# Kernel optimization log

Measured on AMD Instinct MI355X. Metric: run time of the kernel, lower is better.

The kernel has to match this reference:

```python
import jax, jax.numpy as jnp
import numpy as np

N_NODES = 100000
N_EDGES = 1600000
N_FEAT = 32
HIDDEN = 96
N_GRAPHS = 2048


def setup_inputs() -> dict:
    key = jax.random.key(0)
    ks = jax.random.split(key, 16)
    x = jax.random.normal(ks[0], (N_NODES, N_FEAT), dtype=jnp.float32)
    edge_index = jax.random.randint(ks[1], (2, N_EDGES), 0, N_NODES, dtype=jnp.int64)
    batch = jnp.sort(jax.random.randint(ks[2], (N_NODES,), 0, N_GRAPHS, dtype=jnp.int64))

    def glorot(k, shape):
        lim = np.sqrt(6.0 / (shape[0] + shape[1]))
        return jax.random.uniform(k, shape, dtype=jnp.float32, minval=-lim, maxval=lim)

    return {
        "x": x, "edge_index": edge_index, "batch": batch,
        "W1": glorot(ks[3], (N_FEAT, HIDDEN)), "b1": jnp.zeros((HIDDEN,), jnp.float32),
        "W2": glorot(ks[4], (HIDDEN, HIDDEN)), "b2": jnp.zeros((HIDDEN,), jnp.float32),
        "W3": glorot(ks[5], (HIDDEN, HIDDEN)), "b3": jnp.zeros((HIDDEN,), jnp.float32),
        "W4": glorot(ks[6], (HIDDEN, HIDDEN)), "b4": jnp.zeros((HIDDEN,), jnp.float32),
        "Wf1": glorot(ks[7], (HIDDEN, 32)), "bf1": jnp.zeros((32,), jnp.float32),
        "Wf2": glorot(ks[8], (32, 1)), "bf2": jnp.zeros((1,), jnp.float32),
    }


def _gcn_norm(edge_index, num_nodes):
    # PyG GCNConv default: add self-loops, symmetric normalization D^-1/2 (A+I) D^-1/2
    loops = jnp.arange(num_nodes, dtype=edge_index.dtype)
    src = jnp.concatenate([edge_index[0], loops])
    dst = jnp.concatenate([edge_index[1], loops])
    deg = jax.ops.segment_sum(jnp.ones_like(dst, dtype=jnp.float32), dst, num_segments=num_nodes)
    dinv = jnp.where(deg > 0, jax.lax.rsqrt(jnp.where(deg > 0, deg, 1.0)), 0.0)
    norm = dinv[src] * dinv[dst]  # [E + N]
    return src, dst, norm


def _gcn_conv(x, src, dst, norm, W, b, num_nodes):
    xw = x @ W                      # [N, out]
    msg = xw[src] * norm[:, None]   # [E+N, out] gather + scale
    out = jax.ops.segment_sum(msg, dst, num_segments=num_nodes)  # scatter-add
    return out + b


def reference(x, edge_index, batch, W1, b1, W2, b2, W3, b3, W4, b4, Wf1, bf1, Wf2, bf2):
    n = x.shape[0]
    src, dst, norm = _gcn_norm(edge_index, n)
    h = jax.nn.relu(_gcn_conv(x, src, dst, norm, W1, b1, n))
    h = jax.nn.relu(_gcn_conv(h, src, dst, norm, W2, b2, n))
    h = jax.nn.relu(_gcn_conv(h, src, dst, norm, W3, b3, n))
    h = jax.nn.relu(_gcn_conv(h, src, dst, norm, W4, b4, n))
    g = jax.ops.segment_sum(h, batch, num_segments=N_GRAPHS)  # global_add_pool [G, 96]
    g = jax.nn.relu(g @ Wf1 + bf1)
    return g @ Wf2 + bf2  # [G, 1]
```

## Files before the change

### kernel.cpp

```cpp
#include <hip/hip_runtime.h>
#include <hip/hip_fp16.h>


#define HIDDEN 96

__device__ inline float4 h4_to_f4(uint2 u) {
    __half2 a = *reinterpret_cast<__half2*>(&u.x);
    __half2 b = *reinterpret_cast<__half2*>(&u.y);
    float2 fa = __half22float2(a), fb = __half22float2(b);
    return make_float4(fa.x, fa.y, fb.x, fb.y);
}

__device__ inline uint2 f4_to_h4(float4 v) {
    __half2 a = __float22half2_rn(make_float2(v.x, v.y));
    __half2 b = __float22half2_rn(make_float2(v.z, v.w));
    uint2 u;
    u.x = *reinterpret_cast<unsigned*>(&a);
    u.y = *reinterpret_cast<unsigned*>(&b);
    return u;
}

__device__ inline int pad4i(int c) { return (c + 3) & ~3; }

__global__ __launch_bounds__(256) void zero_int_kernel(int* p, int n) {
    int i = blockIdx.x * 256 + threadIdx.x;
    if (i < n) p[i] = 0;
}

__global__ __launch_bounds__(256) void zero_kernel(float* p, int n) {
    int i = blockIdx.x * 256 + threadIdx.x;
    if (i < n) p[i] = 0.0f;
}

__global__ __launch_bounds__(256) void cast_h_kernel(const float4* __restrict__ in,
                                                     uint2* __restrict__ out, int n4) {
    int i = blockIdx.x * 256 + threadIdx.x;
    if (i < n4) out[i] = f4_to_h4(in[i]);
}

__global__ __launch_bounds__(256) void deg_pos_kernel(const int* __restrict__ dst,
                                                      int* __restrict__ cnt,
                                                      int* __restrict__ epos, int E) {
    int e = blockIdx.x * 256 + threadIdx.x;
    if (e < E) epos[e] = atomicAdd(&cnt[dst[e]], 1);
}

__global__ __launch_bounds__(256) void dinv_kernel(const int* __restrict__ cnt,
                                                   float* __restrict__ dinv, int n) {
    int i = blockIdx.x * 256 + threadIdx.x;
    if (i < n) dinv[i] = rsqrtf((float)(cnt[i] + 1));
}

__global__ __launch_bounds__(256) void scan_reduce_kernel(const int* __restrict__ cnt,
                                                          int* __restrict__ bsum, int N) {
    __shared__ int s[256];
    int b = blockIdx.x, tid = threadIdx.x;
    int base = b * 1024;
    int v = 0;
    for (int j = tid; j < 1024; j += 256) {
        int i = base + j;
        v += (i < N) ? pad4i(cnt[i]) : 0;
    }
    s[tid] = v;
    __syncthreads();
    for (int off = 128; off > 0; off >>= 1) {
        if (tid < off) s[tid] += s[tid + off];
        __syncthreads();
    }
    if (tid == 0) bsum[b] = s[0];
}

__global__ __launch_bounds__(128) void scan_bsum_kernel(int* __restrict__ bsum, int nb) {
    __shared__ int s[128];
    int tid = threadIdx.x;
    int v = (tid < nb) ? bsum[tid] : 0;
    s[tid] = v;
    __syncthreads();
    for (int off = 1; off < 128; off <<= 1) {
        int t = (tid >= off) ? s[tid - off] : 0;
        __syncthreads();
        s[tid] += t;
        __syncthreads();
    }
    if (tid < nb) bsum[tid] = s[tid] - v;
}

__global__ __launch_bounds__(256) void scan_write_kernel(const int* __restrict__ cnt,
                                                         const int* __restrict__ bsum,
                                                         int* __restrict__ rowptr, int N) {
    __shared__ int ts[256];
    int b = blockIdx.x, tid = threadIdx.x;
    int base = b * 1024 + tid * 4;
    int v0 = (base + 0 < N) ? pad4i(cnt[base + 0]) : 0;
    int v1 = (base + 1 < N) ? pad4i(cnt[base + 1]) : 0;
    int v2 = (base + 2 < N) ? pad4i(cnt[base + 2]) : 0;
    int v3 = (base + 3 < N) ? pad4i(cnt[base + 3]) : 0;
    int sum = v0 + v1 + v2 + v3;
    ts[tid] = sum;
    __syncthreads();
    for (int off = 1; off < 256; off <<= 1) {
        int t = (tid >= off) ? ts[tid - off] : 0;
        __syncthreads();
        ts[tid] += t;
        __syncthreads();
    }
    int excl = bsum[b] + ts[tid] - sum;
    if (base + 0 <= N) rowptr[base + 0] = excl;
    if (base + 1 <= N) rowptr[base + 1] = excl + v0;
    if (base + 2 <= N) rowptr[base + 2] = excl + v0 + v1;
    if (base + 3 <= N) rowptr[base + 3] = excl + v0 + v1 + v2;
}

__global__ __launch_bounds__(256) void fill_csr_kernel(const int* __restrict__ src,
                                                       const int* __restrict__ dst,
                                                       const int* __restrict__ epos,
                                                       const float* __restrict__ dinv,
                                                       const int* __restrict__ rowptr,
                                                       int* __restrict__ col,
                                                       float* __restrict__ val, int E) {
    int e = blockIdx.x * 256 + threadIdx.x;
    if (e >= E) return;
    int s = src[e];
    int d = dst[e];
    int idx = rowptr[d] + epos[e];
    col[idx] = s;
    val[idx] = dinv[s] * dinv[d];
}

template <int K, bool RELU, bool BIAS>
__global__ __launch_bounds__(256) void gemm_kernel(const uint2* __restrict__ X,
                                                   const float* __restrict__ W,
                                                   const float* __restrict__ b,
                                                   uint2* __restrict__ Y, int n) {
    __shared__ float wlds[K * HIDDEN];
    for (int idx = threadIdx.x; idx < K * HIDDEN; idx += 256) wlds[idx] = W[idx];
    __syncthreads();

    int row = blockIdx.x * 256 + threadIdx.x;
    if (row >= n) return;

    float4 acc[24];
#pragma unroll
    for (int j = 0; j < 24; j++) acc[j] = make_float4(0.f, 0.f, 0.f, 0.f);

    const float4* wl4 = reinterpret_cast<const float4*>(wlds);
    const uint2* xrow = X + (size_t)row * (K / 4);

    for (int k0 = 0; k0 < K; k0 += 4) {
        float4 xv = h4_to_f4(xrow[k0 >> 2]);
        if (RELU) {
            xv.x = fmaxf(xv.x, 0.f); xv.y = fmaxf(xv.y, 0.f);
            xv.z = fmaxf(xv.z, 0.f); xv.w = fmaxf(xv.w, 0.f);
        }
#pragma unroll
        for (int kk = 0; kk < 4; kk++) {
            float xs = (kk == 0) ? xv.x : (kk == 1) ? xv.y : (kk == 2) ? xv.z : xv.w;
#pragma unroll
            for (int j = 0; j < 24; j++) {
                float4 w = wl4[(k0 + kk) * 24 + j];
                acc[j].x += xs * w.x;
                acc[j].y += xs * w.y;
                acc[j].z += xs * w.z;
                acc[j].w += xs * w.w;
            }
        }
    }

    uint2* y2 = Y + (size_t)row * 24;
#pragma unroll
    for (int j = 0; j < 24; j++) {
        if (BIAS) {
            float4 bb = reinterpret_cast<const float4*>(b)[j];
            acc[j].x += bb.x; acc[j].y += bb.y; acc[j].z += bb.z; acc[j].w += bb.w;
        }
        y2[j] = f4_to_h4(acc[j]);
    }
}

template <int TPN, bool POOL, bool BIAS>
__global__ __launch_bounds__(256) void aggregate_kernel(const uint2* __restrict__ xwh,
                                                        const int* __restrict__ rowptr,
                                                        const int* __restrict__ col,
                                                        const float* __restrict__ val,
                                                        const float* __restrict__ dinv,
                                                        const float* __restrict__ b,
                                                        uint2* __restrict__ out,
                                                        const int* __restrict__ batch,
                                                        float* __restrict__ gpool, int n) {
    unsigned t = blockIdx.x * 256 + threadIdx.x;
    unsigned i = t / (unsigned)TPN, q = t % (unsigned)TPN;
    if (i >= (unsigned)n) return;

    float dv = dinv[i];
    float s = dv * dv;
    float4 self = h4_to_f4(xwh[i * TPN + q]);
    float4 acc = make_float4(s * self.x, s * self.y, s * self.z, s * self.w);
    if (BIAS) {
        float4 bb = reinterpret_cast<const float4*>(b)[q];
        acc.x += bb.x; acc.y += bb.y; acc.z += bb.z; acc.w += bb.w;
    }

    int e = rowptr[i], end = rowptr[i + 1];
    for (; e < end; e += 4) {
        int4 c4 = *reinterpret_cast<const int4*>(col + e);
        float4 w4 = *reinterpret_cast<const float4*>(val + e);
        uint2 u0 = xwh[(unsigned)c4.x * TPN + q];
        uint2 u1 = xwh[(unsigned)c4.y * TPN + q];
        uint2 u2 = xwh[(unsigned)c4.z * TPN + q];
        uint2 u3 = xwh[(unsigned)c4.w * TPN + q];
        float4 v0 = h4_to_f4(u0), v1 = h4_to_f4(u1);
        float4 v2 = h4_to_f4(u2), v3 = h4_to_f4(u3);
        acc.x += w4.x * v0.x + w4.y * v1.x + w4.z * v2.x + w4.w * v3.x;
        acc.y += w4.x * v0.y + w4.y * v1.y + w4.z * v2.y + w4.w * v3.y;
        acc.z += w4.x * v0.z + w4.y * v1.z + w4.z * v2.z + w4.w * v3.z;
        acc.w += w4.x * v0.w + w4.y * v1.w + w4.z * v2.w + w4.w * v3.w;
    }

    if (POOL) {
        float* o = gpool + (size_t)batch[i] * (TPN * 4);
        unsigned fo = q * 4u;
        atomicAdd(o + fo + 0, fmaxf(acc.x, 0.f));
        atomicAdd(o + fo + 1, fmaxf(acc.y, 0.f));
        atomicAdd(o + fo + 2, fmaxf(acc.z, 0.f));
        atomicAdd(o + fo + 3, fmaxf(acc.w, 0.f));
    } else {
        out[i * TPN + q] = f4_to_h4(acc);
    }
}

__global__ __launch_bounds__(64) void mlp_kernel(const float* __restrict__ g,
                                                 const float* __restrict__ Wf1,
                                                 const float* __restrict__ bf1,
                                                 const float* __restrict__ Wf2,
                                                 const float* __restrict__ bf2,
                                                 float* __restrict__ out, int G) {
    __shared__ float gs[HIDDEN];
    __shared__ float hid[32];
    int blk = blockIdx.x;
    int lane = threadIdx.x;
    for (int idx = lane; idx < HIDDEN; idx += 64) gs[idx] = g[(size_t)blk * HIDDEN + idx];
    __syncthreads();
    if (lane < 32) {
        float a = bf1[lane];
        for (int k = 0; k < HIDDEN; k++) a = fmaf(gs[k], Wf1[k * 32 + lane], a);
        hid[lane] = fmaxf(a, 0.f);
    }
    __syncthreads();
    if (lane == 0) {
        float o = bf2[0];
        for (int k = 0; k < 32; k++) o = fmaf(hid[k], Wf2[k], o);
        out[blk] = o;
    }
}

extern "C" void kernel_launch(void* const* d_in, const int* in_sizes, int n_in,
                              void* d_out, int out_size, void* d_ws, size_t ws_size,
                              hipStream_t stream) {
    const float* x     = (const float*)d_in[0];
    const int*   ei    = (const int*)d_in[1];
    const int*   batch = (const int*)d_in[2];
    const float* W1 = (const float*)d_in[3];  const float* b1 = (const float*)d_in[4];
    const float* W2 = (const float*)d_in[5];  const float* b2 = (const float*)d_in[6];
    const float* W3 = (const float*)d_in[7];  const float* b3 = (const float*)d_in[8];
    const float* W4 = (const float*)d_in[9];  const float* b4 = (const float*)d_in[10];
    const float* Wf1 = (const float*)d_in[11]; const float* bf1 = (const float*)d_in[12];
    const float* Wf2 = (const float*)d_in[13]; const float* bf2 = (const float*)d_in[14];
    float* out = (float*)d_out;

    int N = in_sizes[0] / 32;
    int E = in_sizes[1] / 2;
    int G = out_size;
    const int* src = ei;
    const int* dst = ei + E;
    int Emax = E + 4 * N;

    char* ws = (char*)d_ws;
    size_t off = 0;
    auto alloc = [&](size_t bytes) -> void* {
        void* p = (void*)(ws + off);
        off += (bytes + 255) & ~(size_t)255;
        return p;
    };
    int*   degcnt = (int*)alloc((size_t)N * 4);
    float* dinv   = (float*)alloc((size_t)N * 4);
    int*   rowptr = (int*)alloc((size_t)(N + 1) * 4);
    int*   bsum   = (int*)alloc((size_t)128 * 4);
    int*   col    = (int*)alloc((size_t)Emax * 4);
    float* val    = (float*)alloc((size_t)Emax * 4);
    int*   epos   = (int*)alloc((size_t)E * 4);
    uint2* xh     = (uint2*)alloc((size_t)N * 32 * 2);
    uint2* aggXh  = (uint2*)alloc((size_t)N * 32 * 2);
    uint2* bufB   = (uint2*)alloc((size_t)N * HIDDEN * 2);
    uint2* bufH   = (uint2*)alloc((size_t)N * HIDDEN * 2);
    float* gbuf   = (float*)alloc((size_t)G * HIDDEN * 4);
    (void)ws_size;

    int gN   = (N + 255) / 256;
    int gE   = (E + 255) / 256;
    int gEm  = (Emax + 255) / 256;
    int gAgg32 = (int)(((long long)N * 8 + 255) / 256);
    int gAgg96 = (int)(((long long)N * 24 + 255) / 256);
    int nb   = (N + 1023) / 1024;

    zero_int_kernel<<<gN, 256, 0, stream>>>(degcnt, N);
    zero_int_kernel<<<gEm, 256, 0, stream>>>(col, Emax);
    zero_kernel<<<gEm, 256, 0, stream>>>(val, Emax);
    deg_pos_kernel<<<gE, 256, 0, stream>>>(dst, degcnt, epos, E);
    dinv_kernel<<<gN, 256, 0, stream>>>(degcnt, dinv, N);
    scan_reduce_kernel<<<nb, 256, 0, stream>>>(degcnt, bsum, N);
    scan_bsum_kernel<<<1, 128, 0, stream>>>(bsum, nb);
    scan_write_kernel<<<nb, 256, 0, stream>>>(degcnt, bsum, rowptr, N);
    fill_csr_kernel<<<gE, 256, 0, stream>>>(src, dst, epos, dinv, rowptr, col, val, E);

    cast_h_kernel<<<(N * 8 + 255) / 256, 256, 0, stream>>>(
        reinterpret_cast<const float4*>(x), xh, N * 8);
    aggregate_kernel<8, false, false><<<gAgg32, 256, 0, stream>>>(
        xh, rowptr, col, val, dinv, nullptr, aggXh, nullptr, nullptr, N);
    gemm_kernel<32, false, true><<<gN, 256, 0, stream>>>(aggXh, W1, b1, bufB, N);

    gemm_kernel<96, true, false><<<gN, 256, 0, stream>>>(bufB, W2, nullptr, bufH, N);
    aggregate_kernel<24, false, true><<<gAgg96, 256, 0, stream>>>(
        bufH, rowptr, col, val, dinv, b2, bufB, nullptr, nullptr, N);

    gemm_kernel<96, true, false><<<gN, 256, 0, stream>>>(bufB, W3, nullptr, bufH, N);
    aggregate_kernel<24, false, true><<<gAgg96, 256, 0, stream>>>(
        bufH, rowptr, col, val, dinv, b3, bufB, nullptr, nullptr, N);

    zero_kernel<<<(G * HIDDEN + 255) / 256, 256, 0, stream>>>(gbuf, G * HIDDEN);
    gemm_kernel<96, true, false><<<gN, 256, 0, stream>>>(bufB, W4, nullptr, bufH, N);
    aggregate_kernel<24, true, true><<<gAgg96, 256, 0, stream>>>(
        bufH, rowptr, col, val, dinv, b4, nullptr, batch, gbuf, N);

    mlp_kernel<<<G, 64, 0, stream>>>(gbuf, Wf1, bf1, Wf2, bf2, out, G);
}
```

Measured before the change: 694.9 us.

## Replace scalar FP32 dense GEMMs with fp16 MFMA kernels and nontemporal CSR loads

Rewrites the per-layer dense transform as a matrix-core kernel using 16x16x32 fp16 MFMA. Each wave computes 16 rows by 96 columns, with W transposed into LDS as fp16. This replaces the per-thread 96-accumulator FMA loop, which had high register pressure and was compute bound. The aggregation kernel also switches its col/val loads and output stores to nontemporal hints to reduce cache pollution. Weights are now rounded to fp16, and the output stores are scattered 2-byte writes, which may coalesce poorly.

```diff
diff --git a/kernel.cpp b/kernel.cpp
--- a/kernel.cpp
+++ b/kernel.cpp
@@ -3,6 +3,12 @@
 
 
 #define HIDDEN 96
+
+typedef __attribute__((ext_vector_type(8))) _Float16 half8;
+typedef __attribute__((ext_vector_type(4))) float floatx4;
+typedef __attribute__((ext_vector_type(4))) int iv4;
+typedef __attribute__((ext_vector_type(4))) float fv4;
+typedef __attribute__((ext_vector_type(2))) unsigned uv2;
 
 __device__ inline float4 h4_to_f4(uint2 u) {
     __half2 a = *reinterpret_cast<__half2*>(&u.x);
@@ -128,52 +134,53 @@
 }
 
 template <int K, bool RELU, bool BIAS>
-__global__ __launch_bounds__(256) void gemm_kernel(const uint2* __restrict__ X,
-                                                   const float* __restrict__ W,
-                                                   const float* __restrict__ b,
-                                                   uint2* __restrict__ Y, int n) {
-    __shared__ float wlds[K * HIDDEN];
-    for (int idx = threadIdx.x; idx < K * HIDDEN; idx += 256) wlds[idx] = W[idx];
-    __syncthreads();
-
-    int row = blockIdx.x * 256 + threadIdx.x;
-    if (row >= n) return;
-
-    float4 acc[24];
-#pragma unroll
-    for (int j = 0; j < 24; j++) acc[j] = make_float4(0.f, 0.f, 0.f, 0.f);
-
-    const float4* wl4 = reinterpret_cast<const float4*>(wlds);
-    const uint2* xrow = X + (size_t)row * (K / 4);
-
-    for (int k0 = 0; k0 < K; k0 += 4) {
-        float4 xv = h4_to_f4(xrow[k0 >> 2]);
+__global__ __launch_bounds__(256) void gemm_mfma_kernel(const _Float16* __restrict__ X,
+                                                        const float* __restrict__ W,
+                                                        const float* __restrict__ b,
+                                                        _Float16* __restrict__ Y, int n) {
+    constexpr int KS = K + 8;
+    __shared__ _Float16 blds[96 * KS];
+    int tid = threadIdx.x;
+    for (int idx = tid; idx < 96 * K; idx += 256) {
+        int nn = idx / K, kk = idx - nn * K;
+        blds[nn * KS + kk] = (_Float16)W[kk * 96 + nn];
+    }
+    __syncthreads();
+
+    int wave = tid >> 6, lane = tid & 63;
+    int m = lane & 15, quad = lane >> 4;
+    int row0 = blockIdx.x * 64 + wave * 16;
+    int rowA = row0 + m;
+    int rowc = (rowA < n) ? rowA : (n - 1);
+
+    floatx4 acc[6];
+#pragma unroll
+    for (int t = 0; t < 6; t++) acc[t] = (floatx4){0.f, 0.f, 0.f, 0.f};
+
+    const _Float16* xrow = X + (size_t)rowc * K;
+#pragma unroll
+    for (int k0 = 0; k0 < K; k0 += 32) {
+        half8 a = *reinterpret_cast<const half8*>(xrow + k0 + quad * 8);
         if (RELU) {
-            xv.x = fmaxf(xv.x, 0.f); xv.y = fmaxf(xv.y, 0.f);
-            xv.z = fmaxf(xv.z, 0.f); xv.w = fmaxf(xv.w, 0.f);
+#pragma unroll
+            for (int j = 0; j < 8; j++) a[j] = (a[j] > (_Float16)0) ? a[j] : (_Float16)0;
         }
 #pragma unroll
-        for (int kk = 0; kk < 4; kk++) {
-            float xs = (kk == 0) ? xv.x : (kk == 1) ? xv.y : (kk == 2) ? xv.z : xv.w;
-#pragma unroll
-            for (int j = 0; j < 24; j++) {
-                float4 w = wl4[(k0 + kk) * 24 + j];
-                acc[j].x += xs * w.x;
-                acc[j].y += xs * w.y;
-                acc[j].z += xs * w.z;
-                acc[j].w += xs * w.w;
-            }
+        for (int t = 0; t < 6; t++) {
+            half8 bf = *reinterpret_cast<const half8*>(
+                blds + (t * 16 + m) * KS + k0 + quad * 8);
+            acc[t] = __builtin_amdgcn_mfma_f32_16x16x32_f16(a, bf, acc[t], 0, 0, 0);
         }
     }
 
-    uint2* y2 = Y + (size_t)row * 24;
-#pragma unroll
-    for (int j = 0; j < 24; j++) {
-        if (BIAS) {
-            float4 bb = reinterpret_cast<const float4*>(b)[j];
-            acc[j].x += bb.x; acc[j].y += bb.y; acc[j].z += bb.z; acc[j].w += bb.w;
+#pragma unroll
+    for (int t = 0; t < 6; t++) {
+        float bb = BIAS ? b[t * 16 + m] : 0.f;
+#pragma unroll
+        for (int r = 0; r < 4; r++) {
+            int rowO = row0 + quad * 4 + r;
+            if (rowO < n) Y[(size_t)rowO * 96 + t * 16 + m] = (_Float16)(acc[t][r] + bb);
         }
-        y2[j] = f4_to_h4(acc[j]);
     }
 }
 
@@ -202,8 +209,8 @@
 
     int e = rowptr[i], end = rowptr[i + 1];
     for (; e < end; e += 4) {
-        int4 c4 = *reinterpret_cast<const int4*>(col + e);
-        float4 w4 = *reinterpret_cast<const float4*>(val + e);
+        iv4 c4 = __builtin_nontemporal_load(reinterpret_cast<const iv4*>(col + e));
+        fv4 w4 = __builtin_nontemporal_load(reinterpret_cast<const fv4*>(val + e));
         uint2 u0 = xwh[(unsigned)c4.x * TPN + q];
         uint2 u1 = xwh[(unsigned)c4.y * TPN + q];
         uint2 u2 = xwh[(unsigned)c4.z * TPN + q];
@@ -224,7 +231,9 @@
         atomicAdd(o + fo + 2, fmaxf(acc.z, 0.f));
         atomicAdd(o + fo + 3, fmaxf(acc.w, 0.f));
     } else {
-        out[i * TPN + q] = f4_to_h4(acc);
+        uint2 h = f4_to_h4(acc);
+        uv2 hv; hv.x = h.x; hv.y = h.y;
+        __builtin_nontemporal_store(hv, reinterpret_cast<uv2*>(out + i * TPN + q));
     }
 }
 
@@ -298,6 +307,7 @@
     int gN   = (N + 255) / 256;
     int gE   = (E + 255) / 256;
     int gEm  = (Emax + 255) / 256;
+    int gGM  = (N + 63) / 64;
     int gAgg32 = (int)(((long long)N * 8 + 255) / 256);
     int gAgg96 = (int)(((long long)N * 24 + 255) / 256);
     int nb   = (N + 1023) / 1024;
@@ -316,18 +326,26 @@
         reinterpret_cast<const float4*>(x), xh, N * 8);
     aggregate_kernel<8, false, false><<<gAgg32, 256, 0, stream>>>(
         xh, rowptr, col, val, dinv, nullptr, aggXh, nullptr, nullptr, N);
-    gemm_kernel<32, false, true><<<gN, 256, 0, stream>>>(aggXh, W1, b1, bufB, N);
-
-    gemm_kernel<96, true, false><<<gN, 256, 0, stream>>>(bufB, W2, nullptr, bufH, N);
+    gemm_mfma_kernel<32, false, true><<<gGM, 256, 0, stream>>>(
+        reinterpret_cast<const _Float16*>(aggXh), W1, b1,
+        reinterpret_cast<_Float16*>(bufB), N);
+
+    gemm_mfma_kernel<96, true, false><<<gGM, 256, 0, stream>>>(
+        reinterpret_cast<const _Float16*>(bufB), W2, nullptr,
+        reinterpret_cast<_Float16*>(bufH), N);
     aggregate_kernel<24, false, true><<<gAgg96, 256, 0, stream>>>(
         bufH, rowptr, col, val, dinv, b2, bufB, nullptr, nullptr, N);
 
-    gemm_kernel<96, true, false><<<gN, 256, 0, stream>>>(bufB, W3, nullptr, bufH, N);
+    gemm_mfma_kernel<96, true, false><<<gGM, 256, 0, stream>>>(
+        reinterpret_cast<const _Float16*>(bufB), W3, nullptr,
+        reinterpret_cast<_Float16*>(bufH), N);
     aggregate_kernel<24, false, true><<<gAgg96, 256, 0, stream>>>(
         bufH, rowptr, col, val, dinv, b3, bufB, nullptr, nullptr, N);
 
     zero_kernel<<<(G * HIDDEN + 255) / 256, 256, 0, stream>>>(gbuf, G * HIDDEN);
-    gemm_kernel<96, true, false><<<gN, 256, 0, stream>>>(bufB, W4, nullptr, bufH, N);
+    gemm_mfma_kernel<96, true, false><<<gGM, 256, 0, stream>>>(
+        reinterpret_cast<const _Float16*>(bufB), W4, nullptr,
+        reinterpret_cast<_Float16*>(bufH), N);
     aggregate_kernel<24, true, true><<<gAgg96, 256, 0, stream>>>(
         bufH, rowptr, col, val, dinv, b4, nullptr, batch, gbuf, N);
 
```

New measurement: 703.0 us. About the same (+1.2%).
